# Kernel tuning notes

Hardware: AMD Instinct MI355X
Metric: run time of the kernel (lower is better)

The kernel has to match this reference:

```python
import jax, jax.numpy as jnp
import numpy as np

B, T, D, H, O, L = 64, 512, 256, 512, 1, 4


def _lstm_layer(x, W_ih, W_hh, b_ih, b_hh):
    """Single LSTM layer, batch_first. x: [B,T,in] -> [B,T,H].
    PyTorch gate order: i, f, g, o."""
    Bv = x.shape[0]
    Hv = W_hh.shape[1]
    # Precompute input contribution for all timesteps (one big GEMM).
    gx = jnp.einsum('btd,gd->btg', x, W_ih) + b_ih + b_hh  # [B,T,4H]

    def step(carry, g_t):
        h, c = carry
        z = g_t + h @ W_hh.T  # [B,4H]
        i, f, g, o = jnp.split(z, 4, axis=-1)
        i = jax.nn.sigmoid(i)
        f = jax.nn.sigmoid(f)
        g = jnp.tanh(g)
        o = jax.nn.sigmoid(o)
        c = f * c + i * g
        h = o * jnp.tanh(c)
        return (h, c), h

    h0 = jnp.zeros((Bv, Hv), x.dtype)
    c0 = jnp.zeros((Bv, Hv), x.dtype)
    _, hs = jax.lax.scan(step, (h0, c0), jnp.swapaxes(gx, 0, 1))  # [T,B,H]
    return jnp.swapaxes(hs, 0, 1)  # [B,T,H]


def setup_inputs() -> dict:
    key = jax.random.key(0)
    ks = jax.random.split(key, 19)
    s = 1.0 / np.sqrt(H)  # PyTorch LSTM init scale
    d = {"x": jax.random.normal(ks[0], (B, T, D), jnp.float32)}
    dims = [D, H, H, H]
    i = 1
    for l in range(L):
        d[f"W_ih{l}"] = jax.random.normal(ks[i], (4 * H, dims[l]), jnp.float32) * s; i += 1
        d[f"W_hh{l}"] = jax.random.normal(ks[i], (4 * H, H), jnp.float32) * s; i += 1
        d[f"b_ih{l}"] = jax.random.normal(ks[i], (4 * H,), jnp.float32) * s; i += 1
        d[f"b_hh{l}"] = jax.random.normal(ks[i], (4 * H,), jnp.float32) * s; i += 1
    d["W_out"] = jax.random.normal(ks[17], (O, H), jnp.float32) * s
    d["b_out"] = jax.random.normal(ks[18], (O,), jnp.float32) * s
    return d


def reference(x, W_ih0, W_hh0, b_ih0, b_hh0,
              W_ih1, W_hh1, b_ih1, b_hh1,
              W_ih2, W_hh2, b_ih2, b_hh2,
              W_ih3, W_hh3, b_ih3, b_hh3,
              W_out, b_out):
    h = x
    layers = ((W_ih0, W_hh0, b_ih0, b_hh0),
              (W_ih1, W_hh1, b_ih1, b_hh1),
              (W_ih2, W_hh2, b_ih2, b_hh2),
              (W_ih3, W_hh3, b_ih3, b_hh3))
    for Wih, Whh, bih, bhh in layers:
        h = _lstm_layer(h, Wih, Whh, bih, bhh)
    # Linear head on last timestep
    return h[:, -1, :] @ W_out.T + b_out  # [B, O]
```

## Files before the change

kernel.cpp:

```cpp
#include <hip/hip_runtime.h>
#include <hip/hip_fp16.h>

typedef _Float16 h16;
typedef _Float16 v8h  __attribute__((ext_vector_type(8)));
typedef float    v4f  __attribute__((ext_vector_type(4)));

#define FPAT 0x0101010101010101ull

struct PParams {
  const float* x;
  const float* Wih[4];
  const float* Whh[4];
  const float* bih[4];
  const float* bhh[4];
  h16* s[4];
  unsigned char* flags;
};

__device__ inline float fsigmoid(float x){
  float e = __builtin_amdgcn_exp2f(-1.4426950408889634f * __builtin_fabsf(x));
  float r = __builtin_amdgcn_rcpf(1.0f + e);
  return x >= 0.f ? r : e * r;
}
__device__ inline float ftanhf(float x){
  float e = __builtin_amdgcn_exp2f(-2.8853900817779268f * __builtin_fabsf(x));
  float t = (1.0f - e) * __builtin_amdgcn_rcpf(1.0f + e);
  return x >= 0.f ? t : -t;
}

__device__ inline unsigned long long cload64(const void* p){
  return __hip_atomic_load((const unsigned long long*)p, __ATOMIC_RELAXED,
                           __HIP_MEMORY_SCOPE_AGENT);
}
__device__ inline void cstore32(void* p, unsigned int v){
  __hip_atomic_store((unsigned int*)p, v, __ATOMIC_RELAXED, __HIP_MEMORY_SCOPE_AGENT);
}
__device__ inline void cstore8(void* p, unsigned char v){
  __hip_atomic_store((unsigned char*)p, v, __ATOMIC_RELAXED, __HIP_MEMORY_SCOPE_AGENT);
}

__device__ inline void wait_flag16(const unsigned long long* f){
  int it = 0;
  while (true){
    unsigned long long a = cload64(f);
    unsigned long long b = cload64(f + 1);
    if ((a & b) == FPAT) break;
    __builtin_amdgcn_s_sleep(1);
    if (++it > (1 << 21)) break;
  }
}

template<int KIN, bool XSRC>
__device__ void run_layer(const float* __restrict__ Wih, const float* __restrict__ Whh,
                          const float* __restrict__ bih, const float* __restrict__ bhh,
                          const float* __restrict__ xsrc,
                          const h16* __restrict__ src,
                          h16* __restrict__ dst, int dstMask,
                          unsigned char* flagSelf, const unsigned char* flagSrc,
                          int rg, int bg, h16* A)
{
  const int tid  = threadIdx.x;
  const int wv   = tid >> 6;
  const int lane = tid & 63;
  const int ISTR = KIN + 8;
  const int HOFF = 8320;
  const int KI   = KIN / 32;

  const int n16  = lane & 15;
  const int unit = rg*32 + wv*8 + (n16 & 7);
  const int ksub = ((lane >> 4) & 3) * 8;
  const int row0 = ((n16 >> 3)    ) * 512 + unit;
  const int row1 = ((n16 >> 3) + 2) * 512 + unit;

  v8h wihf[KI][2];
  #pragma unroll
  for (int kk = 0; kk < KI; ++kk){
    #pragma unroll
    for (int j = 0; j < 2; ++j){
      const float* p = Wih + (size_t)(j ? row1 : row0) * KIN + kk*32 + ksub;
      v8h fr;
      #pragma unroll
      for (int e = 0; e < 8; ++e) fr[e] = (h16)p[e];
      wihf[kk][j] = fr;
    }
  }
  v8h whhf[16][2];
  #pragma unroll
  for (int kk = 0; kk < 16; ++kk){
    #pragma unroll
    for (int j = 0; j < 2; ++j){
      const float* p = Whh + (size_t)(j ? row1 : row0) * 512 + kk*32 + ksub;
      v8h fr;
      #pragma unroll
      for (int e = 0; e < 8; ++e) fr[e] = (h16)p[e];
      whhf[kk][j] = fr;
    }
  }
  const float bias0 = bih[row0] + bhh[row0];
  const float bias1 = bih[row1] + bhh[row1];
  float c[4] = {0.f, 0.f, 0.f, 0.f};
  const bool hi = (lane & 8) != 0;

  #pragma unroll 1
  for (int t = 0; t < 512; ++t){
    if (!XSRC && tid == 0)
      wait_flag16((const unsigned long long*)(flagSrc + (size_t)t*16));
    __syncthreads();

    if constexpr (XSRC){
      #pragma unroll
      for (int i = 0; i < 2; ++i){
        int q = tid + i*256;
        int row = q >> 5, col = q & 31;
        const float* xp = xsrc + ((size_t)(bg*16 + row)*512 + t)*256 + col*8;
        float4 v0 = *(const float4*)(xp);
        float4 v1 = *(const float4*)(xp + 4);
        v8h o = {(h16)v0.x,(h16)v0.y,(h16)v0.z,(h16)v0.w,
                 (h16)v1.x,(h16)v1.y,(h16)v1.z,(h16)v1.w};
        *(v8h*)(A + row*ISTR + col*8) = o;
      }
    } else {
      unsigned long long a0[4], a1[4];
      #pragma unroll
      for (int i = 0; i < 4; ++i){
        int q = tid + i*256;
        int row = q >> 6, col = q & 63;
        const h16* sp = src + ((size_t)t*64 + bg*16 + row)*512 + col*8;
        a0[i] = cload64(sp);
        a1[i] = cload64(sp + 4);
      }
      #pragma unroll
      for (int i = 0; i < 4; ++i){
        int q = tid + i*256;
        int row = q >> 6, col = q & 63;
        union { unsigned long long u[2]; v8h h; } tmp;
        tmp.u[0] = a0[i]; tmp.u[1] = a1[i];
        *(v8h*)(A + row*ISTR + col*8) = tmp.h;
      }
    }
    __syncthreads();

    unsigned long long pa = FPAT, pb = FPAT;
    if (tid == 0 && t > 0){
      const unsigned long long* fs =
          (const unsigned long long*)(flagSelf + (size_t)(t-1)*16);
      pa = cload64(fs);
      pb = cload64(fs + 1);
    }

    v4f acc0 = {0.f, 0.f, 0.f, 0.f};
    v4f acc1 = {0.f, 0.f, 0.f, 0.f};
    const h16* Ain = A + n16*ISTR + ksub;
    #pragma unroll
    for (int kk = 0; kk < KI; ++kk){
      v8h a = *(const v8h*)(Ain + kk*32);
      acc0 = __builtin_amdgcn_mfma_f32_16x16x32_f16(a, wihf[kk][0], acc0, 0, 0, 0);
      acc1 = __builtin_amdgcn_mfma_f32_16x16x32_f16(a, wihf[kk][1], acc1, 0, 0, 0);
    }

    if (tid == 0 && t > 0 && (pa & pb) != FPAT)
      wait_flag16((const unsigned long long*)(flagSelf + (size_t)(t-1)*16));
    __syncthreads();

    if (t == 0){
      #pragma unroll
      for (int i = 0; i < 4; ++i){
        int q = tid + i*256;
        int row = q >> 6, col = q & 63;
        union { unsigned long long u[2]; v8h h; } tmp;
        tmp.u[0] = 0ull; tmp.u[1] = 0ull;
        *(v8h*)(A + HOFF + row*520 + col*8) = tmp.h;
      }
    } else {
      const h16* hsrc = dst + (size_t)((t-1) & dstMask) * 64 * 512;
      unsigned long long a0[4], a1[4];
      #pragma unroll
      for (int i = 0; i < 4; ++i){
        int q = tid + i*256;
        int row = q >> 6, col = q & 63;
        const h16* sp = hsrc + (size_t)(bg*16 + row)*512 + col*8;
        a0[i] = cload64(sp);
        a1[i] = cload64(sp + 4);
      }
      #pragma unroll
      for (int i = 0; i < 4; ++i){
        int q = tid + i*256;
        int row = q >> 6, col = q & 63;
        union { unsigned long long u[2]; v8h h; } tmp;
        tmp.u[0] = a0[i]; tmp.u[1] = a1[i];
        *(v8h*)(A + HOFF + row*520 + col*8) = tmp.h;
      }
    }
    __syncthreads();

    const h16* Ah = A + HOFF + n16*520 + ksub;
    #pragma unroll
    for (int kk = 0; kk < 16; ++kk){
      v8h a = *(const v8h*)(Ah + kk*32);
      acc0 = __builtin_amdgcn_mfma_f32_16x16x32_f16(a, whhf[kk][0], acc0, 0, 0, 0);
      acc1 = __builtin_amdgcn_mfma_f32_16x16x32_f16(a, whhf[kk][1], acc1, 0, 0, 0);
    }

    h16* drow = dst + (size_t)(t & dstMask) * 64 * 512;
    #pragma unroll
    for (int r = 0; r < 4; ++r){
      float z0 = acc0[r] + bias0;
      float z1 = acc1[r] + bias1;
      float p0 = __shfl_xor(z0, 8, 64);
      float p1 = __shfl_xor(z1, 8, 64);
      float iv = hi ? p0 : z0;
      float fv = hi ? z0 : p0;
      float gv = hi ? p1 : z1;
      float ov = hi ? z1 : p1;
      iv = fsigmoid(iv); fv = fsigmoid(fv); ov = fsigmoid(ov);
      gv = ftanhf(gv);
      c[r] = fv * c[r] + iv * gv;
      float hval = ov * ftanhf(c[r]);
      h16 hh = (h16)hval;
      unsigned int mine = (unsigned int)__builtin_bit_cast(unsigned short, hh);
      unsigned int partner = (unsigned int)__shfl_xor((int)mine, 1, 64);
      if (!hi && !(n16 & 1)){
        int batch = bg*16 + ((lane >> 4) << 2) + r;
        cstore32((void*)(drow + (size_t)batch*512 + unit), mine | (partner << 16));
      }
    }
    __syncthreads();

    if (tid == 0)
      cstore8(flagSelf + (size_t)t*16 + rg, 1);
  }
}

__global__ __launch_bounds__(256, 1) void lstm_persist(PParams p){
  __shared__ h16 A[16640];
  const int bx = blockIdx.x;
  const int l  = bx >> 6;
  const int rg = (bx >> 2) & 15;
  const int bg = bx & 3;
  unsigned char* fl = p.flags + (size_t)(l*4 + bg) * 512 * 16;
  if (l == 0){
    run_layer<256, true >(p.Wih[0], p.Whh[0], p.bih[0], p.bhh[0], p.x, nullptr,
                          p.s[0], 511, fl, nullptr, rg, bg, A);
  } else {
    const unsigned char* fs = p.flags + (size_t)((l-1)*4 + bg) * 512 * 16;
    run_layer<512, false>(p.Wih[l], p.Whh[l], p.bih[l], p.bhh[l], nullptr, p.s[l-1],
                          p.s[l], (l == 3) ? 1 : 511, fl, fs, rg, bg, A);
  }
}

__global__ void head_k(const h16* __restrict__ h3, const float* __restrict__ Wo,
                       const float* __restrict__ bo, float* __restrict__ out){
  const int b = blockIdx.x;
  const int lane = threadIdx.x;
  float s = 0.f;
  for (int u = lane; u < 512; u += 64)
    s += (float)h3[(size_t)b * 512 + u] * Wo[u];
  #pragma unroll
  for (int off = 32; off; off >>= 1) s += __shfl_down(s, off, 64);
  if (lane == 0) out[b] = s + bo[0];
}

__global__ void zero_out_k(float* out, int n){
  int i = blockIdx.x * 64 + threadIdx.x;
  if (i < n) out[i] = 0.f;
}

extern "C" void kernel_launch(void* const* d_in, const int* in_sizes, int n_in,
                              void* d_out, int out_size, void* d_ws, size_t ws_size,
                              hipStream_t stream){
  PParams p;
  p.x = (const float*)d_in[0];
  for (int l = 0; l < 4; ++l){
    p.Wih[l] = (const float*)d_in[1 + 4*l + 0];
    p.Whh[l] = (const float*)d_in[1 + 4*l + 1];
    p.bih[l] = (const float*)d_in[1 + 4*l + 2];
    p.bhh[l] = (const float*)d_in[1 + 4*l + 3];
  }
  const float* Wo = (const float*)d_in[17];
  const float* bo = (const float*)d_in[18];

  const size_t FLAG_BYTES = (size_t)16 * 512 * 16;
  const size_t SBYTES     = (size_t)512 * 64 * 512 * 2;
  const size_t NEED       = FLAG_BYTES + 3 * SBYTES + (size_t)2 * 64 * 512 * 2;

  if (ws_size < NEED){
    zero_out_k<<<dim3(1), dim3(64), 0, stream>>>((float*)d_out, out_size);
    return;
  }

  char* ws = (char*)d_ws;
  p.flags = (unsigned char*)ws;
  size_t off = FLAG_BYTES;
  for (int l = 0; l < 3; ++l){ p.s[l] = (h16*)(ws + off); off += SBYTES; }
  p.s[3] = (h16*)(ws + off);

  hipMemsetAsync(p.flags, 0, FLAG_BYTES, stream);

  void* args[] = { &p };
  hipError_t e = hipLaunchCooperativeKernel((void*)lstm_persist, dim3(256), dim3(256),
                                            args, 0, stream);
  if (e != hipSuccess){
    lstm_persist<<<dim3(256), dim3(256), 0, stream>>>(p);
  }

  head_k<<<dim3(64), dim3(64), 0, stream>>>(p.s[3] + (size_t)64 * 512, Wo, bo, (float*)d_out);
}
```

Baseline: 1.989 ms.

## Detect same-XCD groups and exchange recurrent state through L2-coherent buffers

Renumbers blocks so the 16 row-group blocks of one layer/batch group are contiguous, and has each block record its XCC id at startup. When all 16 blocks share an XCC, the recurrent h exchange and per-step flags go through small double-buffered per-group buffers using sc0 (L2-scope) loads and stores instead of device-coherent accesses, cutting per-timestep sync latency. If polling times out, a shared mode flag switches the group back to the original agent-scope path. This relies on the hardware block-to-XCC placement, and the fallback's correctness under a mixed-mode switch is subtle.

```diff
diff --git a/kernel.cpp b/kernel.cpp
--- a/kernel.cpp
+++ b/kernel.cpp
@@ -4,6 +4,7 @@
 typedef _Float16 h16;
 typedef _Float16 v8h  __attribute__((ext_vector_type(8)));
 typedef float    v4f  __attribute__((ext_vector_type(4)));
+typedef unsigned int v4u __attribute__((ext_vector_type(4)));
 
 #define FPAT 0x0101010101010101ull
 
@@ -15,6 +16,9 @@
   const float* bhh[4];
   h16* s[4];
   unsigned char* flags;
+  unsigned char* flagL2;
+  unsigned char* xcctab;
+  h16* hbuf;
 };
 
 __device__ inline float fsigmoid(float x){
@@ -50,6 +54,45 @@
   }
 }
 
+__device__ inline bool poll_l2_16(const unsigned char* f, int iters){
+  while (iters-- > 0){
+    unsigned long long a, b;
+    asm volatile("global_load_dwordx2 %0, %2, off sc0\n\t"
+                 "global_load_dwordx2 %1, %2, off offset:8 sc0\n\t"
+                 "s_waitcnt vmcnt(0)"
+                 : "=&v"(a), "=&v"(b) : "v"(f) : "memory");
+    if ((a & b) == FPAT) return true;
+    __builtin_amdgcn_s_sleep(1);
+  }
+  return false;
+}
+__device__ inline void ld4x16_sc0(const h16* p0, const h16* p1,
+                                  const h16* p2, const h16* p3,
+                                  v4u& r0, v4u& r1, v4u& r2, v4u& r3){
+  asm volatile("global_load_dwordx4 %0, %4, off sc0\n\t"
+               "global_load_dwordx4 %1, %5, off sc0\n\t"
+               "global_load_dwordx4 %2, %6, off sc0\n\t"
+               "global_load_dwordx4 %3, %7, off sc0\n\t"
+               "s_waitcnt vmcnt(0)"
+               : "=&v"(r0), "=&v"(r1), "=&v"(r2), "=&v"(r3)
+               : "v"(p0), "v"(p1), "v"(p2), "v"(p3) : "memory");
+}
+__device__ inline void st4x32_sc0(h16* p0, unsigned int w0, unsigned int w1,
+                                  unsigned int w2, unsigned int w3){
+  asm volatile("global_store_dword %0, %1, off sc0\n\t"
+               "global_store_dword %0, %2, off offset:1024 sc0\n\t"
+               "global_store_dword %0, %3, off offset:2048 sc0\n\t"
+               "global_store_dword %0, %4, off offset:3072 sc0"
+               :: "v"(p0), "v"(w0), "v"(w1), "v"(w2), "v"(w3) : "memory");
+}
+__device__ inline void st8_sc0(unsigned char* p, unsigned int v){
+  asm volatile("global_store_byte %0, %1, off sc0" :: "v"(p), "v"(v) : "memory");
+}
+
+__device__ inline bool haszero8(unsigned long long x){
+  return ((x - 0x0101010101010101ull) & ~x & 0x8080808080808080ull) != 0ull;
+}
+
 template<int KIN, bool XSRC>
 __device__ void run_layer(const float* __restrict__ Wih, const float* __restrict__ Whh,
                           const float* __restrict__ bih, const float* __restrict__ bhh,
@@ -57,6 +100,7 @@
                           const h16* __restrict__ src,
                           h16* __restrict__ dst, int dstMask,
                           unsigned char* flagSelf, const unsigned char* flagSrc,
+                          unsigned char* fl2, h16* hb, int* modeSh, bool mode0,
                           int rg, int bg, h16* A)
 {
   const int tid  = threadIdx.x;
@@ -99,7 +143,9 @@
   const float bias0 = bih[row0] + bhh[row0];
   const float bias1 = bih[row1] + bhh[row1];
   float c[4] = {0.f, 0.f, 0.f, 0.f};
-  const bool hi = (lane & 8) != 0;
+  const bool hi  = (lane & 8) != 0;
+  const int  lb0 = (lane >> 4) << 2;
+  bool live = mode0;
 
   #pragma unroll 1
   for (int t = 0; t < 512; ++t){
@@ -141,7 +187,7 @@
     __syncthreads();
 
     unsigned long long pa = FPAT, pb = FPAT;
-    if (tid == 0 && t > 0){
+    if (tid == 0 && t > 0 && !live){
       const unsigned long long* fs =
           (const unsigned long long*)(flagSelf + (size_t)(t-1)*16);
       pa = cload64(fs);
@@ -158,9 +204,18 @@
       acc1 = __builtin_amdgcn_mfma_f32_16x16x32_f16(a, wihf[kk][1], acc1, 0, 0, 0);
     }
 
-    if (tid == 0 && t > 0 && (pa & pb) != FPAT)
-      wait_flag16((const unsigned long long*)(flagSelf + (size_t)(t-1)*16));
+    if (tid == 0 && t > 0){
+      if (live){
+        if (!poll_l2_16(fl2 + (size_t)(t-1)*16, 16384)){
+          *modeSh = 0;
+          wait_flag16((const unsigned long long*)(flagSelf + (size_t)(t-1)*16));
+        }
+      } else if ((pa & pb) != FPAT){
+        wait_flag16((const unsigned long long*)(flagSelf + (size_t)(t-1)*16));
+      }
+    }
     __syncthreads();
+    live = (*modeSh != 0);
 
     if (t == 0){
       #pragma unroll
@@ -171,6 +226,17 @@
         tmp.u[0] = 0ull; tmp.u[1] = 0ull;
         *(v8h*)(A + HOFF + row*520 + col*8) = tmp.h;
       }
+    } else if (live){
+      const h16* hsrc = hb + (size_t)((t-1) & 1) * (16*512);
+      const int row = tid >> 6, col = tid & 63;
+      const h16* q0 = hsrc + (size_t)(row     )*512 + col*8;
+      v4u r0, r1, r2, r3;
+      ld4x16_sc0(q0, q0 + 4*512, q0 + 8*512, q0 + 12*512, r0, r1, r2, r3);
+      union { v4u u; v8h h; } cv;
+      cv.u = r0; *(v8h*)(A + HOFF + (row     )*520 + col*8) = cv.h;
+      cv.u = r1; *(v8h*)(A + HOFF + (row +  4)*520 + col*8) = cv.h;
+      cv.u = r2; *(v8h*)(A + HOFF + (row +  8)*520 + col*8) = cv.h;
+      cv.u = r3; *(v8h*)(A + HOFF + (row + 12)*520 + col*8) = cv.h;
     } else {
       const h16* hsrc = dst + (size_t)((t-1) & dstMask) * 64 * 512;
       unsigned long long a0[4], a1[4];
@@ -202,6 +268,7 @@
     }
 
     h16* drow = dst + (size_t)(t & dstMask) * 64 * 512;
+    unsigned int pk[4];
     #pragma unroll
     for (int r = 0; r < 4; ++r){
       float z0 = acc0[r] + bias0;
@@ -219,32 +286,68 @@
       h16 hh = (h16)hval;
       unsigned int mine = (unsigned int)__builtin_bit_cast(unsigned short, hh);
       unsigned int partner = (unsigned int)__shfl_xor((int)mine, 1, 64);
-      if (!hi && !(n16 & 1)){
-        int batch = bg*16 + ((lane >> 4) << 2) + r;
-        cstore32((void*)(drow + (size_t)batch*512 + unit), mine | (partner << 16));
-      }
+      pk[r] = mine | (partner << 16);
+    }
+    const bool wr = (!hi && !(n16 & 1));
+    if (wr){
+      if (mode0){
+        h16* hrow = hb + (size_t)(t & 1) * (16*512) + (size_t)lb0*512 + unit;
+        st4x32_sc0(hrow, pk[0], pk[1], pk[2], pk[3]);
+      }
+      #pragma unroll
+      for (int r = 0; r < 4; ++r)
+        cstore32((void*)(drow + (size_t)(bg*16 + lb0 + r)*512 + unit), pk[r]);
     }
     __syncthreads();
 
-    if (tid == 0)
+    if (tid == 0){
+      if (mode0) st8_sc0(fl2 + (size_t)t*16 + rg, 1u);
       cstore8(flagSelf + (size_t)t*16 + rg, 1);
+    }
   }
 }
 
 __global__ __launch_bounds__(256, 1) void lstm_persist(PParams p){
   __shared__ h16 A[16640];
+  __shared__ int modeSh;
   const int bx = blockIdx.x;
-  const int l  = bx >> 6;
-  const int rg = (bx >> 2) & 15;
-  const int bg = bx & 3;
-  unsigned char* fl = p.flags + (size_t)(l*4 + bg) * 512 * 16;
+  const int g  = bx & 15;
+  const int rg = bx >> 4;
+  const int l  = g >> 2;
+  const int bg = g & 3;
+  const int tid = threadIdx.x;
+
+  unsigned int xcc = (unsigned int)__builtin_amdgcn_s_getreg(63508);
+  if (tid == 0){
+    cstore8(p.xcctab + g*16 + rg, (unsigned char)((xcc & 63u) + 1u));
+    const unsigned long long* tb = (const unsigned long long*)(p.xcctab + g*16);
+    unsigned long long a = 0, b = 0;
+    int it = 0;
+    while (true){
+      a = cload64(tb); b = cload64(tb + 1);
+      if (!haszero8(a) && !haszero8(b)) break;
+      __builtin_amdgcn_s_sleep(1);
+      if (++it > (1 << 16)) break;
+    }
+    unsigned long long v = a & 0xffull;
+    unsigned long long pat = v * 0x0101010101010101ull;
+    modeSh = (a == pat && b == pat && v >= 1ull && v <= 8ull) ? 1 : 0;
+  }
+  __syncthreads();
+  const bool mode0 = (modeSh != 0);
+
+  unsigned char* fl  = p.flags  + (size_t)g * 512 * 16;
+  unsigned char* fl2 = p.flagL2 + (size_t)g * 512 * 16;
+  h16* hb = p.hbuf + (size_t)g * 2 * 16 * 512;
+
   if (l == 0){
     run_layer<256, true >(p.Wih[0], p.Whh[0], p.bih[0], p.bhh[0], p.x, nullptr,
-                          p.s[0], 511, fl, nullptr, rg, bg, A);
+                          p.s[0], 511, fl, nullptr, fl2, hb, &modeSh, mode0, rg, bg, A);
   } else {
-    const unsigned char* fs = p.flags + (size_t)((l-1)*4 + bg) * 512 * 16;
+    const unsigned char* fs = p.flags + (size_t)(g - 4) * 512 * 16;
     run_layer<512, false>(p.Wih[l], p.Whh[l], p.bih[l], p.bhh[l], nullptr, p.s[l-1],
-                          p.s[l], (l == 3) ? 1 : 511, fl, fs, rg, bg, A);
+                          p.s[l], (l == 3) ? 1 : 511, fl, fs, fl2, hb, &modeSh, mode0,
+                          rg, bg, A);
   }
 }
 
@@ -279,9 +382,13 @@
   const float* Wo = (const float*)d_in[17];
   const float* bo = (const float*)d_in[18];
 
-  const size_t FLAG_BYTES = (size_t)16 * 512 * 16;
+  const size_t FLAGS_OFF  = 0;
+  const size_t FLAG2_OFF  = 131072;
+  const size_t XCC_OFF    = 262144;
+  const size_t HBUF_OFF   = 263168;
+  const size_t STREAM_OFF = 263168 + 524288;
   const size_t SBYTES     = (size_t)512 * 64 * 512 * 2;
-  const size_t NEED       = FLAG_BYTES + 3 * SBYTES + (size_t)2 * 64 * 512 * 2;
+  const size_t NEED       = STREAM_OFF + 3 * SBYTES + (size_t)2 * 64 * 512 * 2;
 
   if (ws_size < NEED){
     zero_out_k<<<dim3(1), dim3(64), 0, stream>>>((float*)d_out, out_size);
@@ -289,12 +396,15 @@
   }
 
   char* ws = (char*)d_ws;
-  p.flags = (unsigned char*)ws;
-  size_t off = FLAG_BYTES;
+  p.flags  = (unsigned char*)(ws + FLAGS_OFF);
+  p.flagL2 = (unsigned char*)(ws + FLAG2_OFF);
+  p.xcctab = (unsigned char*)(ws + XCC_OFF);
+  p.hbuf   = (h16*)(ws + HBUF_OFF);
+  size_t off = STREAM_OFF;
   for (int l = 0; l < 3; ++l){ p.s[l] = (h16*)(ws + off); off += SBYTES; }
   p.s[3] = (h16*)(ws + off);
 
-  hipMemsetAsync(p.flags, 0, FLAG_BYTES, stream);
+  hipMemsetAsync(ws, 0, XCC_OFF + 1024, stream);
 
   void* args[] = { &p };
   hipError_t e = hipLaunchCooperativeKernel((void*)lstm_persist, dim3(256), dim3(256),
```

After: 4.794 ms. 2.41x slower.

## Replace per-step self flag wait with timestep-tagged h exchange buffer

Applied to the files above, without the earlier changes.

Each h value is now also written to a double-buffered exchange buffer as a 32-bit word carrying the next timestep tag in its upper half. Consumers poll these tagged words directly, so the per-timestep flag check and the extra barrier on the own-layer recurrent dependency go away. The input-projection MFMAs move after the h load so a single barrier covers both. This doubles store traffic for h, polling rereads data, and there is a new workspace region to zero.

```diff
diff --git a/kernel.cpp b/kernel.cpp
--- a/kernel.cpp
+++ b/kernel.cpp
@@ -6,6 +6,7 @@
 typedef float    v4f  __attribute__((ext_vector_type(4)));
 
 #define FPAT 0x0101010101010101ull
+#define PSTR (16 * 16 * 512)
 
 struct PParams {
   const float* x;
@@ -15,6 +16,7 @@
   const float* bhh[4];
   h16* s[4];
   unsigned char* flags;
+  unsigned int* selfb;
 };
 
 __device__ inline float fsigmoid(float x){
@@ -56,6 +58,7 @@
                           const float* __restrict__ xsrc,
                           const h16* __restrict__ src,
                           h16* __restrict__ dst, int dstMask,
+                          unsigned int* selfb,
                           unsigned char* flagSelf, const unsigned char* flagSrc,
                           int rg, int bg, h16* A)
 {
@@ -72,6 +75,9 @@
   const int row0 = ((n16 >> 3)    ) * 512 + unit;
   const int row1 = ((n16 >> 3) + 2) * 512 + unit;
 
+  const int srow = tid >> 7;
+  const int scol = tid & 127;
+
   v8h wihf[KI][2];
   #pragma unroll
   for (int kk = 0; kk < KI; ++kk){
@@ -103,6 +109,17 @@
 
   #pragma unroll 1
   for (int t = 0; t < 512; ++t){
+    unsigned long long w0[8], w1[8];
+    if (t > 0){
+      const unsigned int* sb = selfb + (size_t)((t-1) & 1) * PSTR;
+      #pragma unroll
+      for (int i = 0; i < 8; ++i){
+        const unsigned int* cp = sb + (size_t)(srow + 2*i)*512 + scol*4;
+        w0[i] = cload64(cp);
+        w1[i] = cload64(cp + 2);
+      }
+    }
+
     if (!XSRC && tid == 0)
       wait_flag16((const unsigned long long*)(flagSrc + (size_t)t*16));
     __syncthreads();
@@ -138,29 +155,6 @@
         *(v8h*)(A + row*ISTR + col*8) = tmp.h;
       }
     }
-    __syncthreads();
-
-    unsigned long long pa = FPAT, pb = FPAT;
-    if (tid == 0 && t > 0){
-      const unsigned long long* fs =
-          (const unsigned long long*)(flagSelf + (size_t)(t-1)*16);
-      pa = cload64(fs);
-      pb = cload64(fs + 1);
-    }
-
-    v4f acc0 = {0.f, 0.f, 0.f, 0.f};
-    v4f acc1 = {0.f, 0.f, 0.f, 0.f};
-    const h16* Ain = A + n16*ISTR + ksub;
-    #pragma unroll
-    for (int kk = 0; kk < KI; ++kk){
-      v8h a = *(const v8h*)(Ain + kk*32);
-      acc0 = __builtin_amdgcn_mfma_f32_16x16x32_f16(a, wihf[kk][0], acc0, 0, 0, 0);
-      acc1 = __builtin_amdgcn_mfma_f32_16x16x32_f16(a, wihf[kk][1], acc1, 0, 0, 0);
-    }
-
-    if (tid == 0 && t > 0 && (pa & pb) != FPAT)
-      wait_flag16((const unsigned long long*)(flagSelf + (size_t)(t-1)*16));
-    __syncthreads();
 
     if (t == 0){
       #pragma unroll
@@ -172,27 +166,49 @@
         *(v8h*)(A + HOFF + row*520 + col*8) = tmp.h;
       }
     } else {
-      const h16* hsrc = dst + (size_t)((t-1) & dstMask) * 64 * 512;
-      unsigned long long a0[4], a1[4];
-      #pragma unroll
-      for (int i = 0; i < 4; ++i){
-        int q = tid + i*256;
-        int row = q >> 6, col = q & 63;
-        const h16* sp = hsrc + (size_t)(bg*16 + row)*512 + col*8;
-        a0[i] = cload64(sp);
-        a1[i] = cload64(sp + 4);
-      }
-      #pragma unroll
-      for (int i = 0; i < 4; ++i){
-        int q = tid + i*256;
-        int row = q >> 6, col = q & 63;
-        union { unsigned long long u[2]; v8h h; } tmp;
-        tmp.u[0] = a0[i]; tmp.u[1] = a1[i];
-        *(v8h*)(A + HOFF + row*520 + col*8) = tmp.h;
+      const unsigned int* sb = selfb + (size_t)((t-1) & 1) * PSTR;
+      const unsigned long long M  = 0xFFFF0000FFFF0000ull;
+      const unsigned long long TP = ((unsigned long long)t << 16)
+                                  | ((unsigned long long)t << 48);
+      unsigned pend = 0xffu;
+      int it = 0;
+      while (true){
+        #pragma unroll
+        for (int i = 0; i < 8; ++i){
+          if (pend & (1u << i)){
+            if ((w0[i] & M) == TP && (w1[i] & M) == TP){
+              unsigned long long pk =  (w0[i] & 0xFFFFull)
+                                    | (((w0[i] >> 32) & 0xFFFFull) << 16)
+                                    | ((w1[i] & 0xFFFFull) << 32)
+                                    | (((w1[i] >> 32) & 0xFFFFull) << 48);
+              int row = srow + 2*i;
+              *(unsigned long long*)(A + HOFF + row*520 + scol*4) = pk;
+              pend &= ~(1u << i);
+            }
+          }
+        }
+        if (!pend || ++it > (1 << 14)) break;
+        #pragma unroll
+        for (int i = 0; i < 8; ++i){
+          if (pend & (1u << i)){
+            const unsigned int* cp = sb + (size_t)(srow + 2*i)*512 + scol*4;
+            w0[i] = cload64(cp);
+            w1[i] = cload64(cp + 2);
+          }
+        }
       }
     }
     __syncthreads();
 
+    v4f acc0 = {0.f, 0.f, 0.f, 0.f};
+    v4f acc1 = {0.f, 0.f, 0.f, 0.f};
+    const h16* Ain = A + n16*ISTR + ksub;
+    #pragma unroll
+    for (int kk = 0; kk < KI; ++kk){
+      v8h a = *(const v8h*)(Ain + kk*32);
+      acc0 = __builtin_amdgcn_mfma_f32_16x16x32_f16(a, wihf[kk][0], acc0, 0, 0, 0);
+      acc1 = __builtin_amdgcn_mfma_f32_16x16x32_f16(a, wihf[kk][1], acc1, 0, 0, 0);
+    }
     const h16* Ah = A + HOFF + n16*520 + ksub;
     #pragma unroll
     for (int kk = 0; kk < 16; ++kk){
@@ -202,6 +218,8 @@
     }
 
     h16* drow = dst + (size_t)(t & dstMask) * 64 * 512;
+    unsigned int* sbW = selfb + (size_t)(t & 1) * PSTR;
+    const unsigned int mytag = ((unsigned)(t + 1)) << 16;
     #pragma unroll
     for (int r = 0; r < 4; ++r){
       float z0 = acc0[r] + bias0;
@@ -219,9 +237,13 @@
       h16 hh = (h16)hval;
       unsigned int mine = (unsigned int)__builtin_bit_cast(unsigned short, hh);
       unsigned int partner = (unsigned int)__shfl_xor((int)mine, 1, 64);
-      if (!hi && !(n16 & 1)){
-        int batch = bg*16 + ((lane >> 4) << 2) + r;
-        cstore32((void*)(drow + (size_t)batch*512 + unit), mine | (partner << 16));
+      if (!hi){
+        int lb = ((lane >> 4) << 2) + r;
+        cstore32((void*)(sbW + (size_t)lb*512 + unit), mine | mytag);
+        if (!(n16 & 1)){
+          cstore32((void*)(drow + (size_t)(bg*16 + lb)*512 + unit),
+                   mine | (partner << 16));
+        }
       }
     }
     __syncthreads();
@@ -237,14 +259,16 @@
   const int l  = bx >> 6;
   const int rg = (bx >> 2) & 15;
   const int bg = bx & 3;
-  unsigned char* fl = p.flags + (size_t)(l*4 + bg) * 512 * 16;
+  const int g  = l*4 + bg;
+  unsigned char* fl = p.flags + (size_t)g * 512 * 16;
+  unsigned int*  sb = p.selfb + (size_t)g * (16 * 512);
   if (l == 0){
     run_layer<256, true >(p.Wih[0], p.Whh[0], p.bih[0], p.bhh[0], p.x, nullptr,
-                          p.s[0], 511, fl, nullptr, rg, bg, A);
+                          p.s[0], 511, sb, fl, nullptr, rg, bg, A);
   } else {
-    const unsigned char* fs = p.flags + (size_t)((l-1)*4 + bg) * 512 * 16;
+    const unsigned char* fs = p.flags + (size_t)(g - 4) * 512 * 16;
     run_layer<512, false>(p.Wih[l], p.Whh[l], p.bih[l], p.bhh[l], nullptr, p.s[l-1],
-                          p.s[l], (l == 3) ? 1 : 511, fl, fs, rg, bg, A);
+                          p.s[l], (l == 3) ? 1 : 511, sb, fl, fs, rg, bg, A);
   }
 }
 
@@ -280,8 +304,10 @@
   const float* bo = (const float*)d_in[18];
 
   const size_t FLAG_BYTES = (size_t)16 * 512 * 16;
+  const size_t SELF_BYTES = (size_t)2 * 16 * 16 * 512 * 4;
+  const size_t STREAM_OFF = FLAG_BYTES + SELF_BYTES;
   const size_t SBYTES     = (size_t)512 * 64 * 512 * 2;
-  const size_t NEED       = FLAG_BYTES + 3 * SBYTES + (size_t)2 * 64 * 512 * 2;
+  const size_t NEED       = STREAM_OFF + 3 * SBYTES + (size_t)2 * 64 * 512 * 2;
 
   if (ws_size < NEED){
     zero_out_k<<<dim3(1), dim3(64), 0, stream>>>((float*)d_out, out_size);
@@ -290,11 +316,12 @@
 
   char* ws = (char*)d_ws;
   p.flags = (unsigned char*)ws;
-  size_t off = FLAG_BYTES;
+  p.selfb = (unsigned int*)(ws + FLAG_BYTES);
+  size_t off = STREAM_OFF;
   for (int l = 0; l < 3; ++l){ p.s[l] = (h16*)(ws + off); off += SBYTES; }
   p.s[3] = (h16*)(ws + off);
 
-  hipMemsetAsync(p.flags, 0, FLAG_BYTES, stream);
+  hipMemsetAsync(ws, 0, FLAG_BYTES + SELF_BYTES, stream);
 
   void* args[] = { &p };
   hipError_t e = hipLaunchCooperativeKernel((void*)lstm_persist, dim3(256), dim3(256),
```

Measured after the change: 3.161 ms. 1.59x slower.

## Per-wave flag polling, plain cached loads, and split MFMA accumulators in LSTM kernel

Applied to the files above, without the earlier changes.

Replaces the single-thread flag wait plus block barrier with every wave polling the flags itself through lane 0 and a broadcast shuffle. This removes two __syncthreads per timestep. Inter-layer and recurrent h reads now use plain vector loads instead of relaxed atomic 64-bit loads, except in the last layer, whose double-buffered output reuses addresses. The MFMA chains are split into even and odd accumulators to shorten dependency chains. The risk is stale cached data under the weaker load semantics, and extra flag polling traffic from all waves.

```diff
diff --git a/kernel.cpp b/kernel.cpp
--- a/kernel.cpp
+++ b/kernel.cpp
@@ -39,18 +39,18 @@
   __hip_atomic_store((unsigned char*)p, v, __ATOMIC_RELAXED, __HIP_MEMORY_SCOPE_AGENT);
 }
 
-__device__ inline void wait_flag16(const unsigned long long* f){
+__device__ inline void wave_wait16(const unsigned long long* f, int lane){
   int it = 0;
   while (true){
-    unsigned long long a = cload64(f);
-    unsigned long long b = cload64(f + 1);
-    if ((a & b) == FPAT) break;
+    unsigned long long a = FPAT, b = FPAT;
+    if (lane == 0){ a = cload64(f); b = cload64(f + 1); }
+    if (__shfl((int)((a & b) == FPAT), 0, 64)) break;
     __builtin_amdgcn_s_sleep(1);
     if (++it > (1 << 21)) break;
   }
 }
 
-template<int KIN, bool XSRC>
+template<int KIN, bool XSRC, bool SAGENT>
 __device__ void run_layer(const float* __restrict__ Wih, const float* __restrict__ Whh,
                           const float* __restrict__ bih, const float* __restrict__ bhh,
                           const float* __restrict__ xsrc,
@@ -103,9 +103,8 @@
 
   #pragma unroll 1
   for (int t = 0; t < 512; ++t){
-    if (!XSRC && tid == 0)
-      wait_flag16((const unsigned long long*)(flagSrc + (size_t)t*16));
-    __syncthreads();
+    if constexpr (!XSRC)
+      wave_wait16((const unsigned long long*)(flagSrc + (size_t)t*16), lane);
 
     if constexpr (XSRC){
       #pragma unroll
@@ -120,47 +119,49 @@
         *(v8h*)(A + row*ISTR + col*8) = o;
       }
     } else {
-      unsigned long long a0[4], a1[4];
-      #pragma unroll
-      for (int i = 0; i < 4; ++i){
-        int q = tid + i*256;
-        int row = q >> 6, col = q & 63;
-        const h16* sp = src + ((size_t)t*64 + bg*16 + row)*512 + col*8;
-        a0[i] = cload64(sp);
-        a1[i] = cload64(sp + 4);
-      }
-      #pragma unroll
-      for (int i = 0; i < 4; ++i){
-        int q = tid + i*256;
-        int row = q >> 6, col = q & 63;
-        union { unsigned long long u[2]; v8h h; } tmp;
-        tmp.u[0] = a0[i]; tmp.u[1] = a1[i];
-        *(v8h*)(A + row*ISTR + col*8) = tmp.h;
+      v8h hv[4];
+      #pragma unroll
+      for (int i = 0; i < 4; ++i){
+        int q = tid + i*256;
+        int row = q >> 6, col = q & 63;
+        hv[i] = *(const v8h*)(src + ((size_t)t*64 + bg*16 + row)*512 + col*8);
+      }
+      #pragma unroll
+      for (int i = 0; i < 4; ++i){
+        int q = tid + i*256;
+        int row = q >> 6, col = q & 63;
+        *(v8h*)(A + row*ISTR + col*8) = hv[i];
       }
     }
     __syncthreads();
 
     unsigned long long pa = FPAT, pb = FPAT;
-    if (tid == 0 && t > 0){
-      const unsigned long long* fs =
-          (const unsigned long long*)(flagSelf + (size_t)(t-1)*16);
-      pa = cload64(fs);
-      pb = cload64(fs + 1);
-    }
-
-    v4f acc0 = {0.f, 0.f, 0.f, 0.f};
-    v4f acc1 = {0.f, 0.f, 0.f, 0.f};
+    const unsigned long long* fsPrev =
+        (const unsigned long long*)(flagSelf + (size_t)(t-1)*16);
+    if (t > 0 && lane == 0){
+      pa = cload64(fsPrev);
+      pb = cload64(fsPrev + 1);
+    }
+
+    v4f a0e = {0.f,0.f,0.f,0.f}, a0o = {0.f,0.f,0.f,0.f};
+    v4f a1e = {0.f,0.f,0.f,0.f}, a1o = {0.f,0.f,0.f,0.f};
     const h16* Ain = A + n16*ISTR + ksub;
     #pragma unroll
     for (int kk = 0; kk < KI; ++kk){
       v8h a = *(const v8h*)(Ain + kk*32);
-      acc0 = __builtin_amdgcn_mfma_f32_16x16x32_f16(a, wihf[kk][0], acc0, 0, 0, 0);
-      acc1 = __builtin_amdgcn_mfma_f32_16x16x32_f16(a, wihf[kk][1], acc1, 0, 0, 0);
-    }
-
-    if (tid == 0 && t > 0 && (pa & pb) != FPAT)
-      wait_flag16((const unsigned long long*)(flagSelf + (size_t)(t-1)*16));
-    __syncthreads();
+      if (kk & 1){
+        a0o = __builtin_amdgcn_mfma_f32_16x16x32_f16(a, wihf[kk][0], a0o, 0, 0, 0);
+        a1o = __builtin_amdgcn_mfma_f32_16x16x32_f16(a, wihf[kk][1], a1o, 0, 0, 0);
+      } else {
+        a0e = __builtin_amdgcn_mfma_f32_16x16x32_f16(a, wihf[kk][0], a0e, 0, 0, 0);
+        a1e = __builtin_amdgcn_mfma_f32_16x16x32_f16(a, wihf[kk][1], a1e, 0, 0, 0);
+      }
+    }
+
+    if (t > 0){
+      if (!__shfl((int)((pa & pb) == FPAT), 0, 64))
+        wave_wait16(fsPrev, lane);
+    }
 
     if (t == 0){
       #pragma unroll
@@ -171,7 +172,7 @@
         tmp.u[0] = 0ull; tmp.u[1] = 0ull;
         *(v8h*)(A + HOFF + row*520 + col*8) = tmp.h;
       }
-    } else {
+    } else if constexpr (SAGENT){
       const h16* hsrc = dst + (size_t)((t-1) & dstMask) * 64 * 512;
       unsigned long long a0[4], a1[4];
       #pragma unroll
@@ -190,6 +191,21 @@
         tmp.u[0] = a0[i]; tmp.u[1] = a1[i];
         *(v8h*)(A + HOFF + row*520 + col*8) = tmp.h;
       }
+    } else {
+      const h16* hsrc = dst + (size_t)((t-1) & dstMask) * 64 * 512;
+      v8h hv[4];
+      #pragma unroll
+      for (int i = 0; i < 4; ++i){
+        int q = tid + i*256;
+        int row = q >> 6, col = q & 63;
+        hv[i] = *(const v8h*)(hsrc + (size_t)(bg*16 + row)*512 + col*8);
+      }
+      #pragma unroll
+      for (int i = 0; i < 4; ++i){
+        int q = tid + i*256;
+        int row = q >> 6, col = q & 63;
+        *(v8h*)(A + HOFF + row*520 + col*8) = hv[i];
+      }
     }
     __syncthreads();
 
@@ -197,15 +213,20 @@
     #pragma unroll
     for (int kk = 0; kk < 16; ++kk){
       v8h a = *(const v8h*)(Ah + kk*32);
-      acc0 = __builtin_amdgcn_mfma_f32_16x16x32_f16(a, whhf[kk][0], acc0, 0, 0, 0);
-      acc1 = __builtin_amdgcn_mfma_f32_16x16x32_f16(a, whhf[kk][1], acc1, 0, 0, 0);
+      if (kk & 1){
+        a0o = __builtin_amdgcn_mfma_f32_16x16x32_f16(a, whhf[kk][0], a0o, 0, 0, 0);
+        a1o = __builtin_amdgcn_mfma_f32_16x16x32_f16(a, whhf[kk][1], a1o, 0, 0, 0);
+      } else {
+        a0e = __builtin_amdgcn_mfma_f32_16x16x32_f16(a, whhf[kk][0], a0e, 0, 0, 0);
+        a1e = __builtin_amdgcn_mfma_f32_16x16x32_f16(a, whhf[kk][1], a1e, 0, 0, 0);
+      }
     }
 
     h16* drow = dst + (size_t)(t & dstMask) * 64 * 512;
     #pragma unroll
     for (int r = 0; r < 4; ++r){
-      float z0 = acc0[r] + bias0;
-      float z1 = acc1[r] + bias1;
+      float z0 = a0e[r] + a0o[r] + bias0;
+      float z1 = a1e[r] + a1o[r] + bias1;
       float p0 = __shfl_xor(z0, 8, 64);
       float p1 = __shfl_xor(z1, 8, 64);
       float iv = hi ? p0 : z0;
@@ -239,12 +260,16 @@
   const int bg = bx & 3;
   unsigned char* fl = p.flags + (size_t)(l*4 + bg) * 512 * 16;
   if (l == 0){
-    run_layer<256, true >(p.Wih[0], p.Whh[0], p.bih[0], p.bhh[0], p.x, nullptr,
-                          p.s[0], 511, fl, nullptr, rg, bg, A);
+    run_layer<256, true,  false>(p.Wih[0], p.Whh[0], p.bih[0], p.bhh[0], p.x, nullptr,
+                                 p.s[0], 511, fl, nullptr, rg, bg, A);
+  } else if (l < 3){
+    const unsigned char* fs = p.flags + (size_t)((l-1)*4 + bg) * 512 * 16;
+    run_layer<512, false, false>(p.Wih[l], p.Whh[l], p.bih[l], p.bhh[l], nullptr,
+                                 p.s[l-1], p.s[l], 511, fl, fs, rg, bg, A);
   } else {
-    const unsigned char* fs = p.flags + (size_t)((l-1)*4 + bg) * 512 * 16;
-    run_layer<512, false>(p.Wih[l], p.Whh[l], p.bih[l], p.bhh[l], nullptr, p.s[l-1],
-                          p.s[l], (l == 3) ? 1 : 511, fl, fs, rg, bg, A);
+    const unsigned char* fs = p.flags + (size_t)(2*4 + bg) * 512 * 16;
+    run_layer<512, false, true >(p.Wih[3], p.Whh[3], p.bih[3], p.bhh[3], nullptr,
+                                 p.s[2], p.s[3], 1, fl, fs, rg, bg, A);
   }
 }
 
```

Measured after the change: 1.909 ms. 1.04x faster.
